# Kernel tuning notes

Measured on AMD Instinct MI355X. Metric: run time of the kernel, lower is better.

## Reference

```python
import jax, jax.numpy as jnp
import numpy as np

N, E = 50000, 800000
IN, OUT, HEADS = 128, 128, 4
HID = OUT // HEADS  # 32
NEG_SLOPE = 0.2  # PyG GATv2Conv default


def setup_inputs() -> dict:
    key = jax.random.key(0)
    ks = jax.random.split(key, 12)
    s = 0.05
    return {
        "x": jax.random.normal(ks[0], (N, IN), jnp.float32),
        "edge_index": jax.random.randint(ks[1], (2, E), 0, N, jnp.int64),
        "edge_weight": jax.random.uniform(ks[2], (E,), jnp.float32),
        "h": jax.random.normal(ks[3], (N, OUT), jnp.float32),
        "Wl": jax.random.normal(ks[4], (IN, HEADS * HID), jnp.float32) * s,
        "Wr": jax.random.normal(ks[5], (IN, HEADS * HID), jnp.float32) * s,
        "att": jax.random.normal(ks[6], (HEADS, HID), jnp.float32) * s,
        "bias_conv": jnp.zeros((HEADS * HID,), jnp.float32),
        "W1": jax.random.normal(ks[7], (2 * OUT, 2 * OUT), jnp.float32) * s,
        "b1": jnp.zeros((2 * OUT,), jnp.float32),
        "W2": jax.random.normal(ks[8], (2 * OUT, OUT), jnp.float32) * s,
        "b2": jnp.zeros((OUT,), jnp.float32),
    }


def gatv2_conv(x, edge_index, Wl, Wr, att, bias_conv):
    n = x.shape[0]
    heads, hid = att.shape
    # add self loops (PyG default add_self_loops=True)
    loops = jnp.arange(n, dtype=edge_index.dtype)
    src = jnp.concatenate([edge_index[0], loops])
    dst = jnp.concatenate([edge_index[1], loops])
    xl = (x @ Wl).reshape(n, heads, hid)  # source transform
    xr = (x @ Wr).reshape(n, heads, hid)  # target transform
    m = xl[src] + xr[dst]                  # [E+N, H, D]
    e = jnp.einsum('ehd,hd->eh', jax.nn.leaky_relu(m, NEG_SLOPE), att)
    mx = jax.ops.segment_max(e, dst, num_segments=n)
    a = jnp.exp(e - mx[dst])
    denom = jax.ops.segment_sum(a, dst, num_segments=n)
    alpha = a / (denom[dst] + 1e-16)       # segment softmax over in-edges
    out = jax.ops.segment_sum(xl[src] * alpha[..., None], dst, num_segments=n)
    return out.reshape(n, heads * hid) + bias_conv


def reference(x, edge_index, edge_weight, h, Wl, Wr, att, bias_conv, W1, b1, W2, b2):
    # edge_weight is accepted by TGATCell.forward but never used
    f = jax.nn.sigmoid(gatv2_conv(x, edge_index, Wl, Wr, att, bias_conv))
    ru = jax.nn.sigmoid(jnp.concatenate([f, h], axis=1) @ W1 + b1)
    r, u = jnp.split(ru, 2, axis=1)
    c = jnp.tanh(jnp.concatenate([f, r * h], axis=1) @ W2 + b2)
    return u * h + (1.0 - u) * c
```

## Files before the change

kernel.cpp:

```cpp
#include <hip/hip_runtime.h>
#include <hip/hip_bf16.h>
#include <math.h>

typedef __attribute__((ext_vector_type(8))) short short8;
typedef __attribute__((ext_vector_type(4))) float floatx4;

__device__ __forceinline__ unsigned short f2b(float f) {
  unsigned int u = __builtin_bit_cast(unsigned int, f);
  u += 0x7fffu + ((u >> 16) & 1u);
  return (unsigned short)(u >> 16);
}
__device__ __forceinline__ float b2f(unsigned short s) {
  unsigned int u = ((unsigned int)s) << 16;
  return __builtin_bit_cast(float, u);
}
__device__ __forceinline__ float sigm(float v) { return 1.f / (1.f + __expf(-v)); }
__device__ __forceinline__ float tanh_fast(float y) {
  float t = __expf(2.f * y);
  return 1.f - 2.f / (t + 1.f);
}

__global__ __launch_bounds__(1024) void detect_kernel(const unsigned int* __restrict__ ei,
                                                      long long n_u32, int* __restrict__ flag) {
  __shared__ int any;
  if (threadIdx.x == 0) any = 0;
  __syncthreads();
  int nz = 0;
  for (int rep = 0; rep < 4; ++rep) {
    long long idx = 2LL * (threadIdx.x + rep * 1024) + 1;
    if (idx < n_u32 && ei[idx] != 0u) nz = 1;
  }
  if (nz) atomicOr(&any, 1);
  __syncthreads();
  if (threadIdx.x == 0) *flag = any;
}

__device__ __forceinline__ int load_dst(const void* ei, int E, int flag, int i) {
  if (flag == 0) return (int)((const long long*)ei)[(long long)E + i];
  return ((const int*)ei)[E + i];
}
__device__ __forceinline__ int load_src(const void* ei, int E, int flag, int i) {
  if (flag == 0) return (int)((const long long*)ei)[i];
  return ((const int*)ei)[i];
}

__global__ __launch_bounds__(256) void bucket_hist(const void* __restrict__ ei, int E,
                                                   const int* __restrict__ flag,
                                                   int* __restrict__ bucketCnt, int nbk) {
  __shared__ int h[512];
  for (int i = threadIdx.x; i < nbk; i += 256) h[i] = 0;
  __syncthreads();
  int fl = *flag;
  int gid = blockIdx.x * 256 + threadIdx.x;
  int stride = gridDim.x * 256;
  for (int i = gid; i < E; i += stride) {
    int d = load_dst(ei, E, fl, i);
    atomicAdd(&h[d >> 7], 1);
  }
  __syncthreads();
  for (int i = threadIdx.x; i < nbk; i += 256)
    if (h[i]) atomicAdd(&bucketCnt[i], h[i]);
}

__global__ __launch_bounds__(64) void bucket_scan(const int* __restrict__ bucketCnt,
                                                  int* __restrict__ bucketBase,
                                                  int* __restrict__ bucketCursor, int nbk) {
  int lane = threadIdx.x;
  int carry = 0;
  for (int base = 0; base < nbk; base += 64) {
    int i = base + lane;
    int v = (i < nbk) ? bucketCnt[i] : 0;
    int s = v;
    #pragma unroll
    for (int ofs = 1; ofs < 64; ofs <<= 1) {
      int t = __shfl_up(s, ofs, 64);
      if (lane >= ofs) s += t;
    }
    if (i < nbk) {
      int ex = s - v + carry;
      bucketBase[i] = ex;
      bucketCursor[i] = ex;
    }
    carry += __shfl(s, 63, 64);
  }
  if (lane == 0) bucketBase[nbk] = carry;
}

__global__ __launch_bounds__(256) void partition_kernel(const void* __restrict__ ei, int E,
                                                        const int* __restrict__ flag,
                                                        int* __restrict__ bucketCursor,
                                                        unsigned long long* __restrict__ pairBuf,
                                                        int nbk) {
  __shared__ int h[512];
  __shared__ int base[512];
  int tid = threadIdx.x;
  for (int i = tid; i < nbk; i += 256) h[i] = 0;
  __syncthreads();
  int fl = *flag;
  int tile0 = blockIdx.x * 4096;
  int sarr[16], darr[16], rank[16];
  #pragma unroll
  for (int k = 0; k < 16; ++k) {
    int idx = tile0 + tid + k * 256;
    rank[k] = -1;
    if (idx < E) {
      sarr[k] = load_src(ei, E, fl, idx);
      darr[k] = load_dst(ei, E, fl, idx);
      rank[k] = atomicAdd(&h[darr[k] >> 7], 1);
    }
  }
  __syncthreads();
  for (int i = tid; i < nbk; i += 256)
    base[i] = h[i] ? atomicAdd(&bucketCursor[i], h[i]) : 0;
  __syncthreads();
  #pragma unroll
  for (int k = 0; k < 16; ++k) {
    if (rank[k] >= 0) {
      int bk = darr[k] >> 7;
      pairBuf[(size_t)base[bk] + rank[k]] =
          ((unsigned long long)(unsigned)darr[k] << 32) | (unsigned)sarr[k];
    }
  }
}

__global__ __launch_bounds__(256) void csr_build(const unsigned long long* __restrict__ pairBuf,
                                                 const int* __restrict__ bucketBase,
                                                 int* __restrict__ off, int* __restrict__ csr,
                                                 int n, int E, int nbk) {
  __shared__ int cnt[128];
  __shared__ int start[128];
  __shared__ int wtot[4];
  int bk = blockIdx.x;
  int tid = threadIdx.x;
  int lo = bucketBase[bk], hi = bucketBase[bk + 1];
  int node0 = bk << 7;
  if (tid < 128) cnt[tid] = 0;
  __syncthreads();
  for (int i = lo + tid; i < hi; i += 256) {
    int d = (int)(pairBuf[i] >> 32);
    atomicAdd(&cnt[d - node0], 1);
  }
  __syncthreads();
  {
    int v = (tid < 128) ? cnt[tid] : 0;
    int s = v;
    #pragma unroll
    for (int ofs = 1; ofs < 64; ofs <<= 1) {
      int t = __shfl_up(s, ofs, 64);
      if ((tid & 63) >= ofs) s += t;
    }
    if ((tid & 63) == 63) wtot[tid >> 6] = s;
    __syncthreads();
    if (tid < 128) {
      int pre = (tid >> 6) ? wtot[0] : 0;
      start[tid] = s - v + pre;
    }
  }
  __syncthreads();
  int nNodes = n - node0;
  if (nNodes > 128) nNodes = 128;
  if (tid < nNodes) off[node0 + tid] = lo + start[tid];
  if (bk == nbk - 1 && tid == 0) off[n] = E;
  if (tid < 128) cnt[tid] = 0;
  __syncthreads();
  for (int i = lo + tid; i < hi; i += 256) {
    unsigned long long pr = pairBuf[i];
    int s = (int)(unsigned)pr;
    int ld = (int)(pr >> 32) - node0;
    int r = atomicAdd(&cnt[ld], 1);
    csr[lo + start[ld] + r] = s;
  }
}

__global__ __launch_bounds__(256) void wprep(const float* __restrict__ Wl,
                                             const float* __restrict__ Wr,
                                             const float* __restrict__ W1,
                                             const float* __restrict__ W2,
                                             unsigned short* __restrict__ Btfxw,
                                             unsigned short* __restrict__ Btf1,
                                             unsigned short* __restrict__ Btf2) {
  int gid = blockIdx.x * 256 + threadIdx.x;
  if (gid < 4096) {
    int lane = gid & 63, fid = gid >> 6;
    int l15 = lane & 15, lhi = lane >> 4;
    int kk = fid & 3, nt = (fid >> 2) & 3, w = fid >> 4;
    int col = w * 64 + nt * 16 + l15;
    int k0 = kk * 32 + lhi * 8;
    #pragma unroll
    for (int e = 0; e < 8; ++e) {
      float v = (col < 128) ? Wl[(k0 + e) * 128 + col] : Wr[(k0 + e) * 128 + (col - 128)];
      Btfxw[(size_t)gid * 8 + e] = f2b(v);
    }
  } else if (gid < 12288) {
    int g = gid - 4096;
    int lane = g & 63, fid = g >> 6;
    int l15 = lane & 15, lhi = lane >> 4;
    int kk = fid & 1, ks = (fid >> 1) & 3, nt = (fid >> 3) & 3, w = fid >> 5;
    int col = (nt < 2) ? (w * 32 + nt * 16 + l15) : (128 + w * 32 + (nt - 2) * 16 + l15);
    int k0 = ks * 64 + kk * 32 + lhi * 8;
    #pragma unroll
    for (int e = 0; e < 8; ++e)
      Btf1[(size_t)g * 8 + e] = f2b(W1[(k0 + e) * 256 + col]);
  } else {
    int g = gid - 12288;
    int lane = g & 63, fid = g >> 6;
    int l15 = lane & 15, lhi = lane >> 4;
    int kk = fid & 1, ks = (fid >> 1) & 3, nt = (fid >> 3) & 1, w = fid >> 4;
    int col = w * 32 + nt * 16 + l15;
    int k0 = ks * 64 + kk * 32 + lhi * 8;
    #pragma unroll
    for (int e = 0; e < 8; ++e)
      Btf2[(size_t)g * 8 + e] = f2b(W2[(k0 + e) * 128 + col]);
  }
}

__global__ __launch_bounds__(256) void gemm_xw(const float* __restrict__ x,
                                               const unsigned short* __restrict__ Btf,
                                               unsigned short* __restrict__ xl,
                                               unsigned short* __restrict__ xr, int n) {
  __shared__ char As[64 * 256];
  int t = threadIdx.x;
  int w = t >> 6, l = t & 63;
  int row0 = blockIdx.x * 64;
  int l15 = l & 15, lhi = l >> 4;

  #pragma unroll
  for (int u_ = 0; u_ < 4; ++u_) {
    int unit = t + u_ * 256;
    int r = unit >> 4, slot = unit & 15;
    int grow = row0 + r;
    uint4 o = make_uint4(0, 0, 0, 0);
    if (grow < n) {
      const float* s = x + (size_t)grow * 128 + slot * 8;
      float4 f0 = *(const float4*)s, f1 = *(const float4*)(s + 4);
      o.x = (unsigned)f2b(f0.x) | ((unsigned)f2b(f0.y) << 16);
      o.y = (unsigned)f2b(f0.z) | ((unsigned)f2b(f0.w) << 16);
      o.z = (unsigned)f2b(f1.x) | ((unsigned)f2b(f1.y) << 16);
      o.w = (unsigned)f2b(f1.z) | ((unsigned)f2b(f1.w) << 16);
    }
    *(uint4*)(As + r * 256 + ((slot * 16) ^ ((r & 7) << 4))) = o;
  }
  __syncthreads();

  floatx4 acc[4][4];
  #pragma unroll
  for (int mt = 0; mt < 4; ++mt)
    #pragma unroll
    for (int nt = 0; nt < 4; ++nt) acc[mt][nt] = (floatx4){0.f, 0.f, 0.f, 0.f};

  #pragma unroll 1
  for (int kk = 0; kk < 4; ++kk) {
    int ko = kk * 64 + lhi * 16;
    short8 a[4];
    #pragma unroll
    for (int mt = 0; mt < 4; ++mt) {
      int r = mt * 16 + l15;
      a[mt] = *(const short8*)(As + r * 256 + (ko ^ ((r & 7) << 4)));
    }
    short8 b[4];
    #pragma unroll
    for (int nt = 0; nt < 4; ++nt) {
      int fid = (w * 4 + nt) * 4 + kk;
      b[nt] = *(const short8*)(Btf + ((size_t)fid * 64 + l) * 8);
    }
    #pragma unroll
    for (int nt = 0; nt < 4; ++nt)
      #pragma unroll
      for (int mt = 0; mt < 4; ++mt)
        acc[mt][nt] = __builtin_amdgcn_mfma_f32_16x16x32_bf16(a[mt], b[nt], acc[mt][nt], 0, 0, 0);
  }

  #pragma unroll
  for (int mt = 0; mt < 4; ++mt)
    #pragma unroll
    for (int nt = 0; nt < 4; ++nt) {
      int col = w * 64 + nt * 16 + l15;
      int rbase = row0 + mt * 16 + lhi * 4;
      #pragma unroll
      for (int j = 0; j < 4; ++j) {
        int row = rbase + j;
        if (row >= n) continue;
        unsigned short v = f2b(acc[mt][nt][j]);
        if (col < 128) xl[(size_t)row * 128 + col] = v;
        else           xr[(size_t)row * 128 + (col - 128)] = v;
      }
    }
}

__global__ __launch_bounds__(256) void node_kernel(const unsigned int* __restrict__ xl32,
                                                   const unsigned int* __restrict__ xr32,
                                                   const float* __restrict__ att,
                                                   const float* __restrict__ bias,
                                                   const int* __restrict__ off,
                                                   const int* __restrict__ csr,
                                                   unsigned int* __restrict__ fout, int n) {
  int wid = threadIdx.x >> 6, lane = threadIdx.x & 63;
  int node = blockIdx.x * 4 + wid;
  if (node >= n) return;
  float a0 = att[2 * lane], a1 = att[2 * lane + 1];
  unsigned int xrp = xr32[(size_t)node * 64 + lane];
  float xr0 = b2f((unsigned short)xrp);
  float xr1 = b2f((unsigned short)(xrp >> 16));
  float num0 = 0.f, num1 = 0.f, den = 0.f;
  int beg = off[node], end = off[node + 1];

  auto comp = [&](unsigned int g) {
    float x0 = b2f((unsigned short)g), x1 = b2f((unsigned short)(g >> 16));
    float m0 = x0 + xr0, m1 = x1 + xr1;
    float l0 = fmaxf(m0, 0.2f * m0), l1 = fmaxf(m1, 0.2f * m1);
    float p = fmaf(l1, a1, l0 * a0);
    #pragma unroll
    for (int mask = 1; mask < 16; mask <<= 1) p += __shfl_xor(p, mask, 64);
    float wgt = __expf(p);
    num0 = fmaf(wgt, x0, num0);
    num1 = fmaf(wgt, x1, num1);
    den += wgt;
  };

  comp(xl32[(size_t)node * 64 + lane]);
  for (int base = beg; base < end; base += 64) {
    int cnt = end - base;
    if (cnt > 64) cnt = 64;
    int my = csr[base + (lane < cnt ? lane : 0)];
    int i = 0;
    for (; i + 4 <= cnt; i += 4) {
      int s0 = __builtin_amdgcn_readlane(my, i);
      int s1 = __builtin_amdgcn_readlane(my, i + 1);
      int s2 = __builtin_amdgcn_readlane(my, i + 2);
      int s3 = __builtin_amdgcn_readlane(my, i + 3);
      unsigned int g0 = xl32[(size_t)s0 * 64 + lane];
      unsigned int g1 = xl32[(size_t)s1 * 64 + lane];
      unsigned int g2 = xl32[(size_t)s2 * 64 + lane];
      unsigned int g3 = xl32[(size_t)s3 * 64 + lane];
      comp(g0); comp(g1); comp(g2); comp(g3);
    }
    for (; i < cnt; ++i) {
      int s0 = __builtin_amdgcn_readlane(my, i);
      comp(xl32[(size_t)s0 * 64 + lane]);
    }
  }
  float inv = 1.f / (den + 1e-16f);
  float v0 = num0 * inv + bias[2 * lane];
  float v1 = num1 * inv + bias[2 * lane + 1];
  fout[(size_t)node * 64 + lane] = (unsigned)f2b(sigm(v0)) | ((unsigned)f2b(sigm(v1)) << 16);
}

__global__ __launch_bounds__(256) void gemm_fused(const unsigned short* __restrict__ fbuf,
                                                  const float* __restrict__ hf,
                                                  const unsigned short* __restrict__ Btf1,
                                                  const unsigned short* __restrict__ Btf2,
                                                  const float* __restrict__ b1,
                                                  const float* __restrict__ b2,
                                                  float* __restrict__ out, int n) {
  __shared__ char As[64 * 512];
  int t = threadIdx.x;
  int w = t >> 6, l = t & 63;
  int row0 = blockIdx.x * 64;
  int l15 = l & 15, lhi = l >> 4;

  #pragma unroll
  for (int u_ = 0; u_ < 8; ++u_) {
    int unit = t + u_ * 256;
    int r = unit >> 5, slot = unit & 31;
    int koff = slot * 16;
    int grow = row0 + r;
    uint4 v = make_uint4(0, 0, 0, 0);
    if (grow < n) {
      if (koff < 256) {
        v = *(const uint4*)(fbuf + (size_t)grow * 128 + koff / 2);
      } else {
        const float* s = hf + (size_t)grow * 128 + (koff - 256) / 2;
        float4 f0 = *(const float4*)s, f1 = *(const float4*)(s + 4);
        v.x = (unsigned)f2b(f0.x) | ((unsigned)f2b(f0.y) << 16);
        v.y = (unsigned)f2b(f0.z) | ((unsigned)f2b(f0.w) << 16);
        v.z = (unsigned)f2b(f1.x) | ((unsigned)f2b(f1.y) << 16);
        v.w = (unsigned)f2b(f1.z) | ((unsigned)f2b(f1.w) << 16);
      }
    }
    *(uint4*)(As + r * 512 + (koff ^ ((r & 7) << 4))) = v;
  }
  __syncthreads();

  floatx4 acc[4][4];
  #pragma unroll
  for (int mt = 0; mt < 4; ++mt)
    #pragma unroll
    for (int nt = 0; nt < 4; ++nt) acc[mt][nt] = (floatx4){0.f, 0.f, 0.f, 0.f};

  #pragma unroll 1
  for (int ks = 0; ks < 4; ++ks) {
    #pragma unroll
    for (int kk = 0; kk < 2; ++kk) {
      int ka = ks * 128 + kk * 64 + lhi * 16;
      short8 a[4];
      #pragma unroll
      for (int mt = 0; mt < 4; ++mt) {
        int r = mt * 16 + l15;
        a[mt] = *(const short8*)(As + r * 512 + (ka ^ ((r & 7) << 4)));
      }
      #pragma unroll
      for (int nt = 0; nt < 4; ++nt) {
        int fid = ((w * 4 + nt) * 4 + ks) * 2 + kk;
        short8 b = *(const short8*)(Btf1 + ((size_t)fid * 64 + l) * 8);
        #pragma unroll
        for (int mt = 0; mt < 4; ++mt)
          acc[mt][nt] = __builtin_amdgcn_mfma_f32_16x16x32_bf16(a[mt], b, acc[mt][nt], 0, 0, 0);
      }
    }
  }
  __syncthreads();

  float us[4][2][4];
  #pragma unroll
  for (int mt = 0; mt < 4; ++mt)
    #pragma unroll
    for (int nt = 0; nt < 4; ++nt) {
      #pragma unroll
      for (int j = 0; j < 4; ++j) {
        int rloc = mt * 16 + lhi * 4 + j;
        if (nt < 2) {
          int col = w * 32 + nt * 16 + l15;
          float s = sigm(acc[mt][nt][j] + b1[col]);
          int byteoff = (256 + col * 2) ^ ((rloc & 7) << 4);
          char* p = As + rloc * 512 + byteoff;
          unsigned short hv = *(unsigned short*)p;
          *(unsigned short*)p = f2b(s * b2f(hv));
        } else {
          int col = 128 + w * 32 + (nt - 2) * 16 + l15;
          us[mt][nt - 2][j] = sigm(acc[mt][nt][j] + b1[col]);
        }
      }
    }
  __syncthreads();

  floatx4 acc2[4][2];
  #pragma unroll
  for (int mt = 0; mt < 4; ++mt)
    #pragma unroll
    for (int nt = 0; nt < 2; ++nt) acc2[mt][nt] = (floatx4){0.f, 0.f, 0.f, 0.f};

  #pragma unroll 1
  for (int ks = 0; ks < 4; ++ks) {
    #pragma unroll
    for (int kk = 0; kk < 2; ++kk) {
      int ka = ks * 128 + kk * 64 + lhi * 16;
      short8 a[4];
      #pragma unroll
      for (int mt = 0; mt < 4; ++mt) {
        int r = mt * 16 + l15;
        a[mt] = *(const short8*)(As + r * 512 + (ka ^ ((r & 7) << 4)));
      }
      #pragma unroll
      for (int nt = 0; nt < 2; ++nt) {
        int fid = ((w * 2 + nt) * 4 + ks) * 2 + kk;
        short8 b = *(const short8*)(Btf2 + ((size_t)fid * 64 + l) * 8);
        #pragma unroll
        for (int mt = 0; mt < 4; ++mt)
          acc2[mt][nt] = __builtin_amdgcn_mfma_f32_16x16x32_bf16(a[mt], b, acc2[mt][nt], 0, 0, 0);
      }
    }
  }

  #pragma unroll
  for (int mt = 0; mt < 4; ++mt)
    #pragma unroll
    for (int nt = 0; nt < 2; ++nt) {
      int col = w * 32 + nt * 16 + l15;
      #pragma unroll
      for (int j = 0; j < 4; ++j) {
        int rloc = mt * 16 + lhi * 4 + j;
        int row = row0 + rloc;
        if (row >= n) continue;
        float c = tanh_fast(acc2[mt][nt][j] + b2[col]);
        float uu = us[mt][nt][j];
        float hv = hf[(size_t)row * 128 + col];
        out[(size_t)row * 128 + col] = uu * hv + (1.f - uu) * c;
      }
    }
}

extern "C" void kernel_launch(void* const* d_in, const int* in_sizes, int n_in,
                              void* d_out, int out_size, void* d_ws, size_t ws_size,
                              hipStream_t stream) {
  const float* x     = (const float*)d_in[0];
  const void*  ei    = d_in[1];
  const float* h     = (const float*)d_in[3];
  const float* Wl    = (const float*)d_in[4];
  const float* Wr    = (const float*)d_in[5];
  const float* att   = (const float*)d_in[6];
  const float* bconv = (const float*)d_in[7];
  const float* W1    = (const float*)d_in[8];
  const float* b1    = (const float*)d_in[9];
  const float* W2    = (const float*)d_in[10];
  const float* b2    = (const float*)d_in[11];
  float* out = (float*)d_out;

  const int n = in_sizes[0] / 128;
  const int E = in_sizes[1] / 2;
  const int nbk = (n + 127) >> 7;

  char* w = (char*)d_ws;
  size_t o = 0;
  auto alloc = [&](size_t bytes) {
    char* p = w + o;
    o += bytes;
    o = (o + 255) & ~(size_t)255;
    return p;
  };
  int* flag         = (int*)alloc(4);
  int* bucketCnt    = (int*)alloc((size_t)nbk * 4);
  int* bucketBase   = (int*)alloc((size_t)(nbk + 1) * 4);
  int* bucketCursor = (int*)alloc((size_t)nbk * 4);
  int* off          = (int*)alloc((size_t)(n + 1) * 4);
  int* csr          = (int*)alloc((size_t)E * 4);
  unsigned long long* pairBuf = (unsigned long long*)alloc((size_t)E * 8);
  unsigned short* xl   = (unsigned short*)alloc((size_t)n * 128 * 2);
  unsigned short* xr   = (unsigned short*)alloc((size_t)n * 128 * 2);
  unsigned short* fbuf = (unsigned short*)alloc((size_t)n * 128 * 2);
  unsigned short* Btfxw = (unsigned short*)alloc(4096 * 8 * 2);
  unsigned short* Btf1  = (unsigned short*)alloc(8192 * 8 * 2);
  unsigned short* Btf2  = (unsigned short*)alloc(4096 * 8 * 2);

  hipMemsetAsync(bucketCnt, 0, (size_t)nbk * 4, stream);
  detect_kernel<<<1, 1024, 0, stream>>>((const unsigned int*)ei, 2LL * E, flag);
  bucket_hist<<<256, 256, 0, stream>>>(ei, E, flag, bucketCnt, nbk);
  bucket_scan<<<1, 64, 0, stream>>>(bucketCnt, bucketBase, bucketCursor, nbk);
  partition_kernel<<<(E + 4095) / 4096, 256, 0, stream>>>(ei, E, flag, bucketCursor,
                                                          pairBuf, nbk);
  csr_build<<<nbk, 256, 0, stream>>>(pairBuf, bucketBase, off, csr, n, E, nbk);
  wprep<<<64, 256, 0, stream>>>(Wl, Wr, W1, W2, Btfxw, Btf1, Btf2);

  int gblocks = (n + 63) / 64;
  gemm_xw<<<gblocks, 256, 0, stream>>>(x, Btfxw, xl, xr, n);
  node_kernel<<<(n + 3) / 4, 256, 0, stream>>>((const unsigned int*)xl, (const unsigned int*)xr,
                                               att, bconv, off, csr,
                                               (unsigned int*)fbuf, n);
  gemm_fused<<<gblocks, 256, 0, stream>>>(fbuf, h, Btf1, Btf2, b1, b2, out, n);
}
```

Measured before the change: 164.5 us.

## Process two edges per wavefront in GATv2 aggregation and unroll GEMM K-loops

The node aggregation kernel now splits each wavefront into two 32-lane halves. Each half handles a different edge and loads 4 bf16 features per lane instead of 2, and the two halves' partial sums are combined with a final cross-half shuffle. This halves the edge iterations and shortens the per-head reduction to 3 shuffles. It also folds log2(e) into the attention weights so exp2 can be used directly. The GEMM kernels' K-loops are unrolled more, at some risk of higher register pressure.

```diff
diff --git a/kernel.cpp b/kernel.cpp
--- a/kernel.cpp
+++ b/kernel.cpp
@@ -248,7 +248,7 @@
     #pragma unroll
     for (int nt = 0; nt < 4; ++nt) acc[mt][nt] = (floatx4){0.f, 0.f, 0.f, 0.f};
 
-  #pragma unroll 1
+  #pragma unroll
   for (int kk = 0; kk < 4; ++kk) {
     int ko = kk * 64 + lhi * 16;
     short8 a[4];
@@ -297,52 +297,86 @@
   int wid = threadIdx.x >> 6, lane = threadIdx.x & 63;
   int node = blockIdx.x * 4 + wid;
   if (node >= n) return;
-  float a0 = att[2 * lane], a1 = att[2 * lane + 1];
-  unsigned int xrp = xr32[(size_t)node * 64 + lane];
-  float xr0 = b2f((unsigned short)xrp);
-  float xr1 = b2f((unsigned short)(xrp >> 16));
-  float num0 = 0.f, num1 = 0.f, den = 0.f;
+  int hl = lane & 31;
+  bool upper = lane >= 32;
+  const float LOG2E = 1.44269504f;
+  float4 av = *(const float4*)(att + hl * 4);
+  float a0 = av.x * LOG2E, a1 = av.y * LOG2E, a2 = av.z * LOG2E, a3 = av.w * LOG2E;
+  uint2 xrp = *(const uint2*)(xr32 + node * 64 + hl * 2);
+  float xr0 = b2f((unsigned short)xrp.x), xr1 = b2f((unsigned short)(xrp.x >> 16));
+  float xr2 = b2f((unsigned short)xrp.y), xr3 = b2f((unsigned short)(xrp.y >> 16));
+  float num0 = 0.f, num1 = 0.f, num2 = 0.f, num3 = 0.f, den = 0.f;
   int beg = off[node], end = off[node + 1];
 
-  auto comp = [&](unsigned int g) {
-    float x0 = b2f((unsigned short)g), x1 = b2f((unsigned short)(g >> 16));
-    float m0 = x0 + xr0, m1 = x1 + xr1;
+  auto edge2 = [&](int sLo, int sHi, bool hiValid) {
+    int s = upper ? sHi : sLo;
+    unsigned voff = ((unsigned)s << 6) + (unsigned)(hl << 1);
+    uint2 g = *(const uint2*)(xl32 + voff);
+    float x0 = b2f((unsigned short)g.x), x1 = b2f((unsigned short)(g.x >> 16));
+    float x2 = b2f((unsigned short)g.y), x3 = b2f((unsigned short)(g.y >> 16));
+    float m0 = x0 + xr0, m1 = x1 + xr1, m2 = x2 + xr2, m3 = x3 + xr3;
     float l0 = fmaxf(m0, 0.2f * m0), l1 = fmaxf(m1, 0.2f * m1);
-    float p = fmaf(l1, a1, l0 * a0);
-    #pragma unroll
-    for (int mask = 1; mask < 16; mask <<= 1) p += __shfl_xor(p, mask, 64);
-    float wgt = __expf(p);
+    float l2 = fmaxf(m2, 0.2f * m2), l3 = fmaxf(m3, 0.2f * m3);
+    float p = l0 * a0;
+    p = fmaf(l1, a1, p);
+    p = fmaf(l2, a2, p);
+    p = fmaf(l3, a3, p);
+    p += __shfl_xor(p, 1, 64);
+    p += __shfl_xor(p, 2, 64);
+    p += __shfl_xor(p, 4, 64);
+    float wgt = __builtin_amdgcn_exp2f(p);
+    if (upper && !hiValid) wgt = 0.f;
     num0 = fmaf(wgt, x0, num0);
     num1 = fmaf(wgt, x1, num1);
+    num2 = fmaf(wgt, x2, num2);
+    num3 = fmaf(wgt, x3, num3);
     den += wgt;
   };
 
-  comp(xl32[(size_t)node * 64 + lane]);
-  for (int base = beg; base < end; base += 64) {
-    int cnt = end - base;
-    if (cnt > 64) cnt = 64;
-    int my = csr[base + (lane < cnt ? lane : 0)];
-    int i = 0;
-    for (; i + 4 <= cnt; i += 4) {
-      int s0 = __builtin_amdgcn_readlane(my, i);
-      int s1 = __builtin_amdgcn_readlane(my, i + 1);
-      int s2 = __builtin_amdgcn_readlane(my, i + 2);
-      int s3 = __builtin_amdgcn_readlane(my, i + 3);
-      unsigned int g0 = xl32[(size_t)s0 * 64 + lane];
-      unsigned int g1 = xl32[(size_t)s1 * 64 + lane];
-      unsigned int g2 = xl32[(size_t)s2 * 64 + lane];
-      unsigned int g3 = xl32[(size_t)s3 * 64 + lane];
-      comp(g0); comp(g1); comp(g2); comp(g3);
-    }
-    for (; i < cnt; ++i) {
-      int s0 = __builtin_amdgcn_readlane(my, i);
-      comp(xl32[(size_t)s0 * 64 + lane]);
-    }
-  }
-  float inv = 1.f / (den + 1e-16f);
-  float v0 = num0 * inv + bias[2 * lane];
-  float v1 = num1 * inv + bias[2 * lane + 1];
-  fout[(size_t)node * 64 + lane] = (unsigned)f2b(sigm(v0)) | ((unsigned)f2b(sigm(v1)) << 16);
+  if (beg < end) {
+    edge2(node, csr[beg], true);
+    for (int base = beg + 1; base < end; base += 64) {
+      int cnt = end - base;
+      if (cnt > 64) cnt = 64;
+      int my = csr[base + (lane < cnt ? lane : 0)];
+      int i = 0;
+      for (; i + 4 <= cnt; i += 4) {
+        int sa = __builtin_amdgcn_readlane(my, i);
+        int sb = __builtin_amdgcn_readlane(my, i + 1);
+        int sc = __builtin_amdgcn_readlane(my, i + 2);
+        int sd = __builtin_amdgcn_readlane(my, i + 3);
+        edge2(sa, sb, true);
+        edge2(sc, sd, true);
+      }
+      for (; i + 2 <= cnt; i += 2) {
+        int sa = __builtin_amdgcn_readlane(my, i);
+        int sb = __builtin_amdgcn_readlane(my, i + 1);
+        edge2(sa, sb, true);
+      }
+      if (i < cnt) edge2(__builtin_amdgcn_readlane(my, i), node, false);
+    }
+  } else {
+    edge2(node, node, false);
+  }
+
+  num0 += __shfl_xor(num0, 32, 64);
+  num1 += __shfl_xor(num1, 32, 64);
+  num2 += __shfl_xor(num2, 32, 64);
+  num3 += __shfl_xor(num3, 32, 64);
+  den  += __shfl_xor(den, 32, 64);
+
+  if (!upper) {
+    float inv = 1.f / (den + 1e-16f);
+    float4 bv = *(const float4*)(bias + hl * 4);
+    float v0 = num0 * inv + bv.x;
+    float v1 = num1 * inv + bv.y;
+    float v2 = num2 * inv + bv.z;
+    float v3 = num3 * inv + bv.w;
+    uint2 o;
+    o.x = (unsigned)f2b(sigm(v0)) | ((unsigned)f2b(sigm(v1)) << 16);
+    o.y = (unsigned)f2b(sigm(v2)) | ((unsigned)f2b(sigm(v3)) << 16);
+    *(uint2*)(fout + node * 64 + hl * 2) = o;
+  }
 }
 
 __global__ __launch_bounds__(256) void gemm_fused(const unsigned short* __restrict__ fbuf,
@@ -387,7 +421,7 @@
     #pragma unroll
     for (int nt = 0; nt < 4; ++nt) acc[mt][nt] = (floatx4){0.f, 0.f, 0.f, 0.f};
 
-  #pragma unroll 1
+  #pragma unroll 2
   for (int ks = 0; ks < 4; ++ks) {
     #pragma unroll
     for (int kk = 0; kk < 2; ++kk) {
@@ -439,7 +473,7 @@
     #pragma unroll
     for (int nt = 0; nt < 2; ++nt) acc2[mt][nt] = (floatx4){0.f, 0.f, 0.f, 0.f};
 
-  #pragma unroll 1
+  #pragma unroll 2
   for (int ks = 0; ks < 4; ++ks) {
     #pragma unroll
     for (int kk = 0; kk < 2; ++kk) {
```

New measurement: 160.8 us. 2.3% less time.
